# Performance work log

Measured on AMD Instinct MI355X. Metric: run time of the kernel, lower is better.

The kernel has to match this reference:

```python
import jax, jax.numpy as jnp
import numpy as np

B, NPG, C = 256, 256, 256  # graphs, nodes-per-graph, in_channels
MAX_LEN = 500


def _sinusoid_pe(max_len, c):
    pos = np.arange(max_len, dtype=np.float32)[:, None]
    div = np.exp(np.arange(0, c, 2, dtype=np.float32) * (-np.log(10000.0) / c))
    pe = np.zeros((max_len, c), np.float32)
    pe[:, 0::2] = np.sin(pos * div)
    pe[:, 1::2] = np.cos(pos * div)
    return jnp.asarray(pe)


def setup_inputs() -> dict:
    key = jax.random.key(0)
    ks = jax.random.split(key, 8)
    N = B * NPG
    x = jax.random.normal(ks[0], (N, C), jnp.float32)
    batch = jnp.repeat(jnp.arange(B, dtype=jnp.int32), NPG)
    # every other atom in each graph is an N/O atom -> 128 per graph
    on_index = (jnp.arange(B, dtype=jnp.int32)[:, None] * NPG
                + jnp.arange(0, NPG, 2, dtype=jnp.int32)[None, :]).reshape(-1)
    W1 = jax.random.normal(ks[1], (C, 256), jnp.float32) / np.sqrt(C)
    b1 = jnp.zeros((256,), jnp.float32)
    W2 = jax.random.normal(ks[2], (256, 128), jnp.float32) / np.sqrt(256.0)
    b2 = jnp.zeros((128,), jnp.float32)
    W3 = jax.random.normal(ks[3], (128, 64), jnp.float32) / np.sqrt(128.0)
    b3 = jnp.zeros((64,), jnp.float32)
    w_atom = jax.random.normal(ks[4], (64,), jnp.float32) / 8.0
    return {"x": x, "pe": _sinusoid_pe(MAX_LEN, C), "W1": W1, "b1": b1,
            "W2": W2, "b2": b2, "W3": W3, "b3": b3, "w_atom": w_atom,
            "batch": batch, "on_index": on_index, "ratio": 16}


def _lrelu(z):
    return jnp.where(z > 0, z, 0.1 * z)


def reference(x, pe, W1, b1, W2, b2, W3, b3, w_atom, batch, on_index, ratio):
    N = x.shape[0]
    bsz = int(batch[-1]) + 1
    num_nodes = jax.ops.segment_sum(jnp.ones_like(batch), batch, num_segments=bsz)
    cum = jnp.concatenate([jnp.zeros((1,), batch.dtype), jnp.cumsum(num_nodes)[:-1]])
    n = int(num_nodes.max())  # max_num_nodes
    idx_in_graph = jnp.arange(N, dtype=batch.dtype) - cum[batch]
    # positional encoding (dropout = identity in eval)
    xp = x + pe[idx_in_graph]
    # scoring MLP
    h = _lrelu(xp @ W1 + b1)
    h = _lrelu(h @ W2 + b2)
    h = _lrelu(h @ W3 + b3)
    score = jnp.tanh((h * w_atom).sum(-1) / jnp.linalg.norm(w_atom))
    # dense-pack scores into [bsz, n] padded with -inf, sort descending per row
    dense_idx = jnp.arange(N, dtype=batch.dtype) - cum[batch] + batch * n
    dense = jnp.full((bsz * n,), jnp.finfo(x.dtype).min, x.dtype).at[dense_idx].set(score)
    order = jnp.argsort(-dense.reshape(bsz, n), axis=-1)       # perm within row
    ranks = jnp.argsort(order, axis=-1)                         # inverse perm
    pos_in_perm = (jnp.arange(bsz)[:, None] * n + ranks).reshape(-1)
    # positions (in the flattened perm) of N/O atoms, sorted -> grouped per graph
    on_par = dense_idx[on_index]                                # padded/parallel ids
    indices = jnp.sort(pos_in_perm[on_par])
    m = on_index.shape[0] // bsz                                # N/O atoms per graph (uniform here)
    k = min(int(ratio), m)                                      # k = min(ratio, on_num)
    pre_mask = (jnp.arange(bsz)[:, None] * m + jnp.arange(k)[None, :]).reshape(-1)
    mask = indices[pre_mask]
    # map padded indices back to global node ids (subtract cumulative void counts)
    void = n - num_nodes
    cum_void = jnp.concatenate([jnp.zeros((1,), batch.dtype), jnp.cumsum(void)[:-1]])
    perm_flat = (order + (jnp.arange(bsz) * n - cum_void)[:, None]).reshape(-1)
    perm = perm_flat[mask]
    x_top = (xp[perm] * score[perm][:, None]).reshape(bsz, int(ratio), -1)
    return (x_top, perm, score[on_index], on_index)
```

## Files before the change

kernel.cpp:

```cpp
#include <hip/hip_runtime.h>
#include <hip/hip_bf16.h>


typedef __attribute__((ext_vector_type(8))) short short8v;
typedef __attribute__((ext_vector_type(4))) float float4v;

#define LDA 264

#define W1P_OFF 0
#define W2P_OFF 131072
#define W3P_OFF 196608
#define SCORES_OFF 212992

static __device__ __forceinline__ float lrelu(float z) { return z > 0.0f ? z : 0.1f * z; }

static __device__ __forceinline__ short f2bf(float f) {
    union { float f; unsigned u; } v; v.f = f;
    const unsigned r = v.u + 0x7FFFu + ((v.u >> 16) & 1u);
    return (short)(r >> 16);
}

__global__ __launch_bounds__(256) void pack_kernel(
    const float* __restrict__ W1, const float* __restrict__ W2,
    const float* __restrict__ W3, short* __restrict__ ws)
{
    const int u = blockIdx.x * 256 + threadIdx.x;
    if (u >= 13312) return;
    const float* W; int N, unitBase, uu;
    short* dst;
    if (u < 8192)       { W = W1; N = 256; uu = u;         dst = ws + (W1P_OFF/2); unitBase = 8; }
    else if (u < 12288) { W = W2; N = 128; uu = u - 8192;  dst = ws + (W2P_OFF/2); unitBase = 8; }
    else                { W = W3; N = 64;  uu = u - 12288; dst = ws + (W3P_OFF/2); unitBase = 4; }
    const int perNt = unitBase * 64;
    const int nt   = uu / perNt;
    const int rem  = uu % perNt;
    const int ks   = rem / 64;
    const int lane = rem % 64;
    const int q = lane >> 4;
    const int n = nt * 16 + (lane & 15);
    short8v frag;
    #pragma unroll
    for (int j = 0; j < 8; ++j) {
        const int k = ks * 32 + q * 8 + j;
        frag[j] = f2bf(W[(size_t)k * N + n]);
    }
    *(short8v*)(dst + (size_t)uu * 8) = frag;
}

__global__ __launch_bounds__(256) void mlp_score_kernel(
    const float* __restrict__ x, const float* __restrict__ pe,
    const float* __restrict__ b1, const float* __restrict__ b2,
    const float* __restrict__ b3, const float* __restrict__ w_atom,
    const int* __restrict__ on_index, const short* __restrict__ ws_pack,
    float* __restrict__ ws_scores,
    float* __restrict__ out_score, float* __restrict__ out_onidx)
{
    __shared__ __align__(16) short XP[32 * LDA];
    __shared__ __align__(16) short H1[32 * LDA];
    const int t   = threadIdx.x;
    const int m0  = blockIdx.x * 32;
    const int wid = t >> 6;
    const int lane = t & 63;
    const int q = lane >> 4;
    const int c = lane & 15;

    const short* W1p = ws_pack + (W1P_OFF / 2);
    const short* W2p = ws_pack + (W2P_OFF / 2);
    const short* W3p = ws_pack + (W3P_OFF / 2);

    #pragma unroll
    for (int i = 0; i < 4; ++i) {
        const int u = t + i * 256;
        const int r = u >> 5;
        const int k = (u & 31) << 3;
        const int node = on_index[m0 + r];
        const float4 xa = *(const float4*)(x + (size_t)node * 256 + k);
        const float4 xb = *(const float4*)(x + (size_t)node * 256 + k + 4);
        const float4 pa = *(const float4*)(pe + (size_t)(node & 255) * 256 + k);
        const float4 pb = *(const float4*)(pe + (size_t)(node & 255) * 256 + k + 4);
        short8v s;
        s[0] = f2bf(xa.x + pa.x); s[1] = f2bf(xa.y + pa.y);
        s[2] = f2bf(xa.z + pa.z); s[3] = f2bf(xa.w + pa.w);
        s[4] = f2bf(xb.x + pb.x); s[5] = f2bf(xb.y + pb.y);
        s[6] = f2bf(xb.z + pb.z); s[7] = f2bf(xb.w + pb.w);
        *(short8v*)(&XP[r * LDA + k]) = s;
    }
    __syncthreads();

    {
        const int nt0 = wid * 4;
        float4v acc[2][4];
        #pragma unroll
        for (int nt = 0; nt < 4; ++nt) {
            const float bb = b1[(nt0 + nt) * 16 + c];
            acc[0][nt] = (float4v){bb, bb, bb, bb};
            acc[1][nt] = (float4v){bb, bb, bb, bb};
        }
        #pragma unroll
        for (int ks = 0; ks < 8; ++ks) {
            const short8v a0 = *(const short8v*)(&XP[c * LDA + ks * 32 + q * 8]);
            const short8v a1 = *(const short8v*)(&XP[(16 + c) * LDA + ks * 32 + q * 8]);
            #pragma unroll
            for (int nt = 0; nt < 4; ++nt) {
                const short8v b = *(const short8v*)(W1p + ((size_t)((nt0 + nt) * 8 + ks) * 64 + lane) * 8);
                acc[0][nt] = __builtin_amdgcn_mfma_f32_16x16x32_bf16(a0, b, acc[0][nt], 0, 0, 0);
                acc[1][nt] = __builtin_amdgcn_mfma_f32_16x16x32_bf16(a1, b, acc[1][nt], 0, 0, 0);
            }
        }
        #pragma unroll
        for (int mt = 0; mt < 2; ++mt)
            #pragma unroll
            for (int nt = 0; nt < 4; ++nt)
                #pragma unroll
                for (int r = 0; r < 4; ++r)
                    H1[(mt * 16 + q * 4 + r) * LDA + (nt0 + nt) * 16 + c] = f2bf(lrelu(acc[mt][nt][r]));
    }
    __syncthreads();

    {
        const int nt0 = wid * 2;
        float4v acc[2][2];
        #pragma unroll
        for (int nt = 0; nt < 2; ++nt) {
            const float bb = b2[(nt0 + nt) * 16 + c];
            acc[0][nt] = (float4v){bb, bb, bb, bb};
            acc[1][nt] = (float4v){bb, bb, bb, bb};
        }
        #pragma unroll
        for (int ks = 0; ks < 8; ++ks) {
            const short8v a0 = *(const short8v*)(&H1[c * LDA + ks * 32 + q * 8]);
            const short8v a1 = *(const short8v*)(&H1[(16 + c) * LDA + ks * 32 + q * 8]);
            #pragma unroll
            for (int nt = 0; nt < 2; ++nt) {
                const short8v b = *(const short8v*)(W2p + ((size_t)((nt0 + nt) * 8 + ks) * 64 + lane) * 8);
                acc[0][nt] = __builtin_amdgcn_mfma_f32_16x16x32_bf16(a0, b, acc[0][nt], 0, 0, 0);
                acc[1][nt] = __builtin_amdgcn_mfma_f32_16x16x32_bf16(a1, b, acc[1][nt], 0, 0, 0);
            }
        }
        #pragma unroll
        for (int mt = 0; mt < 2; ++mt)
            #pragma unroll
            for (int nt = 0; nt < 2; ++nt)
                #pragma unroll
                for (int r = 0; r < 4; ++r)
                    XP[(mt * 16 + q * 4 + r) * LDA + (nt0 + nt) * 16 + c] = f2bf(lrelu(acc[mt][nt][r]));
    }
    __syncthreads();

    {
        const int nt = wid;
        float4v acc[2];
        const float bb = b3[nt * 16 + c];
        acc[0] = (float4v){bb, bb, bb, bb};
        acc[1] = (float4v){bb, bb, bb, bb};
        #pragma unroll
        for (int ks = 0; ks < 4; ++ks) {
            const short8v a0 = *(const short8v*)(&XP[c * LDA + ks * 32 + q * 8]);
            const short8v a1 = *(const short8v*)(&XP[(16 + c) * LDA + ks * 32 + q * 8]);
            const short8v b = *(const short8v*)(W3p + ((size_t)(nt * 4 + ks) * 64 + lane) * 8);
            acc[0] = __builtin_amdgcn_mfma_f32_16x16x32_bf16(a0, b, acc[0], 0, 0, 0);
            acc[1] = __builtin_amdgcn_mfma_f32_16x16x32_bf16(a1, b, acc[1], 0, 0, 0);
        }
        float* H3F = (float*)H1;
        #pragma unroll
        for (int mt = 0; mt < 2; ++mt)
            #pragma unroll
            for (int r = 0; r < 4; ++r)
                H3F[(mt * 16 + q * 4 + r) * 66 + nt * 16 + c] = lrelu(acc[mt][r]);
    }
    __syncthreads();

    {
        const float* H3F = (const float*)H1;
        float* PART = (float*)XP;
        const int r = t >> 3, p = t & 7;
        float s = 0.0f;
        #pragma unroll
        for (int j = 0; j < 8; ++j) s += H3F[r * 66 + p * 8 + j] * w_atom[p * 8 + j];
        PART[t] = s;
        __syncthreads();
        if (t < 32) {
            float sum = 0.0f;
            #pragma unroll
            for (int pp = 0; pp < 8; ++pp) sum += PART[t * 8 + pp];
            float n2 = 0.0f;
            for (int cc = 0; cc < 64; ++cc) { const float w = w_atom[cc]; n2 += w * w; }
            const float sc = tanhf(sum / sqrtf(n2));
            const int m = m0 + t;
            ws_scores[m] = sc;
            out_score[m] = sc;
            out_onidx[m] = (float)on_index[m];
        }
    }
}

__global__ __launch_bounds__(256) void topk_gather_kernel(
    const float* __restrict__ x, const float* __restrict__ pe,
    const float* __restrict__ ws_scores, const int* __restrict__ on_index,
    float* __restrict__ out_perm, float* __restrict__ out_xtop)
{
    __shared__ float s[128];
    __shared__ int   sel_node[16];
    __shared__ float sel_sc[16];
    const int g = blockIdx.x, t = threadIdx.x;
    if (t < 128) s[t] = ws_scores[g * 128 + t];
    __syncthreads();
    if (t < 128) {
        const float sj = s[t];
        int rank = 0;
        for (int i = 0; i < 128; ++i) {
            const float si = s[i];
            rank += (si > sj) || (si == sj && i < t);
        }
        if (rank < 16) {
            const int node = on_index[g * 128 + t];
            sel_node[rank] = node;
            sel_sc[rank]   = sj;
            out_perm[g * 16 + rank] = (float)node;
        }
    }
    __syncthreads();
    #pragma unroll
    for (int k = 0; k < 16; ++k) {
        const int node = sel_node[k];
        const float sc = sel_sc[k];
        const float v = (x[(size_t)node * 256 + t] + pe[(size_t)(node & 255) * 256 + t]) * sc;
        out_xtop[((size_t)(g * 16 + k)) * 256 + t] = v;
    }
}

extern "C" void kernel_launch(void* const* d_in, const int* in_sizes, int n_in,
                              void* d_out, int out_size, void* d_ws, size_t ws_size,
                              hipStream_t stream)
{
    const float* x   = (const float*)d_in[0];
    const float* pe  = (const float*)d_in[1];
    const float* W1  = (const float*)d_in[2];
    const float* b1  = (const float*)d_in[3];
    const float* W2  = (const float*)d_in[4];
    const float* b2  = (const float*)d_in[5];
    const float* W3  = (const float*)d_in[6];
    const float* b3  = (const float*)d_in[7];
    const float* wa  = (const float*)d_in[8];
    const int* on_index = (const int*)d_in[10];

    float* out = (float*)d_out;
    float* out_xtop  = out;
    float* out_perm  = out + 1048576;
    float* out_score = out + 1048576 + 4096;
    float* out_onidx = out + 1048576 + 4096 + 32768;

    short* ws_pack   = (short*)d_ws;
    float* ws_scores = (float*)((char*)d_ws + SCORES_OFF);

    hipLaunchKernelGGL(pack_kernel, dim3(52), dim3(256), 0, stream, W1, W2, W3, ws_pack);
    hipLaunchKernelGGL(mlp_score_kernel, dim3(1024), dim3(256), 0, stream,
                       x, pe, b1, b2, b3, wa, on_index, (const short*)ws_pack,
                       ws_scores, out_score, out_onidx);
    hipLaunchKernelGGL(topk_gather_kernel, dim3(256), dim3(256), 0, stream,
                       x, pe, ws_scores, on_index, out_perm, out_xtop);
}
```

Baseline: 126.8 us.

## Swizzle LDS layout, split layer-1 tiles, and raise occupancy hint

Replaces the padded LDS row stride with an XOR-swizzled 256-element layout, shrinking shared memory while keeping MFMA fragment loads free of bank conflicts. Layer 1 is split into two passes of two N-tiles each to cut accumulator register pressure, and launch_bounds now asks for 5 blocks per CU. An extra barrier is added before layer-2 results overwrite XP, and the float scratch stride changes from 66 to 68. The aim is more resident waves to hide gather latency, at the cost of reloading the A fragments twice in layer 1 and one more synchronisation.

```diff
diff --git a/kernel.cpp b/kernel.cpp
--- a/kernel.cpp
+++ b/kernel.cpp
@@ -4,8 +4,6 @@
 
 typedef __attribute__((ext_vector_type(8))) short short8v;
 typedef __attribute__((ext_vector_type(4))) float float4v;
-
-#define LDA 264
 
 #define W1P_OFF 0
 #define W2P_OFF 131072
@@ -18,6 +16,10 @@
     union { float f; unsigned u; } v; v.f = f;
     const unsigned r = v.u + 0x7FFFu + ((v.u >> 16) & 1u);
     return (short)(r >> 16);
+}
+
+static __device__ __forceinline__ int sw_off(int row, int chunk, int within) {
+    return row * 256 + ((chunk ^ (row & 7)) << 3) + within;
 }
 
 __global__ __launch_bounds__(256) void pack_kernel(
@@ -47,7 +49,7 @@
     *(short8v*)(dst + (size_t)uu * 8) = frag;
 }
 
-__global__ __launch_bounds__(256) void mlp_score_kernel(
+__global__ __launch_bounds__(256, 5) void mlp_score_kernel(
     const float* __restrict__ x, const float* __restrict__ pe,
     const float* __restrict__ b1, const float* __restrict__ b2,
     const float* __restrict__ b3, const float* __restrict__ w_atom,
@@ -55,8 +57,8 @@
     float* __restrict__ ws_scores,
     float* __restrict__ out_score, float* __restrict__ out_onidx)
 {
-    __shared__ __align__(16) short XP[32 * LDA];
-    __shared__ __align__(16) short H1[32 * LDA];
+    __shared__ __align__(16) short XP[32 * 256];
+    __shared__ __align__(16) short H1[32 * 256];
     const int t   = threadIdx.x;
     const int m0  = blockIdx.x * 32;
     const int wid = t >> 6;
@@ -72,7 +74,8 @@
     for (int i = 0; i < 4; ++i) {
         const int u = t + i * 256;
         const int r = u >> 5;
-        const int k = (u & 31) << 3;
+        const int ck = u & 31;
+        const int k = ck << 3;
         const int node = on_index[m0 + r];
         const float4 xa = *(const float4*)(x + (size_t)node * 256 + k);
         const float4 xb = *(const float4*)(x + (size_t)node * 256 + k + 4);
@@ -83,26 +86,27 @@
         s[2] = f2bf(xa.z + pa.z); s[3] = f2bf(xa.w + pa.w);
         s[4] = f2bf(xb.x + pb.x); s[5] = f2bf(xb.y + pb.y);
         s[6] = f2bf(xb.z + pb.z); s[7] = f2bf(xb.w + pb.w);
-        *(short8v*)(&XP[r * LDA + k]) = s;
-    }
-    __syncthreads();
-
-    {
-        const int nt0 = wid * 4;
-        float4v acc[2][4];
-        #pragma unroll
-        for (int nt = 0; nt < 4; ++nt) {
-            const float bb = b1[(nt0 + nt) * 16 + c];
+        *(short8v*)(&XP[sw_off(r, ck, 0)]) = s;
+    }
+    __syncthreads();
+
+    #pragma unroll
+    for (int g = 0; g < 2; ++g) {
+        const int ntA = wid * 4 + g * 2;
+        float4v acc[2][2];
+        #pragma unroll
+        for (int nt = 0; nt < 2; ++nt) {
+            const float bb = b1[(ntA + nt) * 16 + c];
             acc[0][nt] = (float4v){bb, bb, bb, bb};
             acc[1][nt] = (float4v){bb, bb, bb, bb};
         }
         #pragma unroll
         for (int ks = 0; ks < 8; ++ks) {
-            const short8v a0 = *(const short8v*)(&XP[c * LDA + ks * 32 + q * 8]);
-            const short8v a1 = *(const short8v*)(&XP[(16 + c) * LDA + ks * 32 + q * 8]);
-            #pragma unroll
-            for (int nt = 0; nt < 4; ++nt) {
-                const short8v b = *(const short8v*)(W1p + ((size_t)((nt0 + nt) * 8 + ks) * 64 + lane) * 8);
+            const short8v a0 = *(const short8v*)(&XP[sw_off(c,      ks * 4 + q, 0)]);
+            const short8v a1 = *(const short8v*)(&XP[sw_off(16 + c, ks * 4 + q, 0)]);
+            #pragma unroll
+            for (int nt = 0; nt < 2; ++nt) {
+                const short8v b = *(const short8v*)(W1p + ((size_t)((ntA + nt) * 8 + ks) * 64 + lane) * 8);
                 acc[0][nt] = __builtin_amdgcn_mfma_f32_16x16x32_bf16(a0, b, acc[0][nt], 0, 0, 0);
                 acc[1][nt] = __builtin_amdgcn_mfma_f32_16x16x32_bf16(a1, b, acc[1][nt], 0, 0, 0);
             }
@@ -110,10 +114,13 @@
         #pragma unroll
         for (int mt = 0; mt < 2; ++mt)
             #pragma unroll
-            for (int nt = 0; nt < 4; ++nt)
+            for (int nt = 0; nt < 2; ++nt)
                 #pragma unroll
-                for (int r = 0; r < 4; ++r)
-                    H1[(mt * 16 + q * 4 + r) * LDA + (nt0 + nt) * 16 + c] = f2bf(lrelu(acc[mt][nt][r]));
+                for (int r = 0; r < 4; ++r) {
+                    const int row = mt * 16 + q * 4 + r;
+                    const int col = (ntA + nt) * 16 + c;
+                    H1[sw_off(row, col >> 3, col & 7)] = f2bf(lrelu(acc[mt][nt][r]));
+                }
     }
     __syncthreads();
 
@@ -128,8 +135,8 @@
         }
         #pragma unroll
         for (int ks = 0; ks < 8; ++ks) {
-            const short8v a0 = *(const short8v*)(&H1[c * LDA + ks * 32 + q * 8]);
-            const short8v a1 = *(const short8v*)(&H1[(16 + c) * LDA + ks * 32 + q * 8]);
+            const short8v a0 = *(const short8v*)(&H1[sw_off(c,      ks * 4 + q, 0)]);
+            const short8v a1 = *(const short8v*)(&H1[sw_off(16 + c, ks * 4 + q, 0)]);
             #pragma unroll
             for (int nt = 0; nt < 2; ++nt) {
                 const short8v b = *(const short8v*)(W2p + ((size_t)((nt0 + nt) * 8 + ks) * 64 + lane) * 8);
@@ -137,13 +144,17 @@
                 acc[1][nt] = __builtin_amdgcn_mfma_f32_16x16x32_bf16(a1, b, acc[1][nt], 0, 0, 0);
             }
         }
+        __syncthreads();
         #pragma unroll
         for (int mt = 0; mt < 2; ++mt)
             #pragma unroll
             for (int nt = 0; nt < 2; ++nt)
                 #pragma unroll
-                for (int r = 0; r < 4; ++r)
-                    XP[(mt * 16 + q * 4 + r) * LDA + (nt0 + nt) * 16 + c] = f2bf(lrelu(acc[mt][nt][r]));
+                for (int r = 0; r < 4; ++r) {
+                    const int row = mt * 16 + q * 4 + r;
+                    const int col = (nt0 + nt) * 16 + c;
+                    XP[sw_off(row, col >> 3, col & 7)] = f2bf(lrelu(acc[mt][nt][r]));
+                }
     }
     __syncthreads();
 
@@ -155,8 +166,8 @@
         acc[1] = (float4v){bb, bb, bb, bb};
         #pragma unroll
         for (int ks = 0; ks < 4; ++ks) {
-            const short8v a0 = *(const short8v*)(&XP[c * LDA + ks * 32 + q * 8]);
-            const short8v a1 = *(const short8v*)(&XP[(16 + c) * LDA + ks * 32 + q * 8]);
+            const short8v a0 = *(const short8v*)(&XP[sw_off(c,      ks * 4 + q, 0)]);
+            const short8v a1 = *(const short8v*)(&XP[sw_off(16 + c, ks * 4 + q, 0)]);
             const short8v b = *(const short8v*)(W3p + ((size_t)(nt * 4 + ks) * 64 + lane) * 8);
             acc[0] = __builtin_amdgcn_mfma_f32_16x16x32_bf16(a0, b, acc[0], 0, 0, 0);
             acc[1] = __builtin_amdgcn_mfma_f32_16x16x32_bf16(a1, b, acc[1], 0, 0, 0);
@@ -166,7 +177,7 @@
         for (int mt = 0; mt < 2; ++mt)
             #pragma unroll
             for (int r = 0; r < 4; ++r)
-                H3F[(mt * 16 + q * 4 + r) * 66 + nt * 16 + c] = lrelu(acc[mt][r]);
+                H3F[(mt * 16 + q * 4 + r) * 68 + nt * 16 + c] = lrelu(acc[mt][r]);
     }
     __syncthreads();
 
@@ -176,7 +187,7 @@
         const int r = t >> 3, p = t & 7;
         float s = 0.0f;
         #pragma unroll
-        for (int j = 0; j < 8; ++j) s += H3F[r * 66 + p * 8 + j] * w_atom[p * 8 + j];
+        for (int j = 0; j < 8; ++j) s += H3F[r * 68 + p * 8 + j] * w_atom[p * 8 + j];
         PART[t] = s;
         __syncthreads();
         if (t < 32) {
```

Measured after the change: 129.7 us. 2.3% more time.
